# Performance work log

Hardware: AMD Instinct MI355X
Metric: run time of the kernel (lower is better)

## Reference

```python
import jax, jax.numpy as jnp
import numpy as np

WP = 1.0     # warp_penalty
TEMP = 0.01  # soft-min temperature
BIG = 1e7    # finite stand-in for +inf (exp(-BIG/TEMP) == 0 exactly in fp32)


def setup_inputs() -> dict:
    key = jax.random.key(0)
    k1, k2, k3, k4 = jax.random.split(key, 4)
    B, T1, T2, C = 8, 256, 1024, 128
    fea_a = jax.random.normal(k1, (B, T1, C), jnp.float32)
    fea_b = jax.random.normal(k2, (B, T2, C), jnp.float32)
    len_a = jax.random.randint(k3, (B,), T1 // 2, T1 + 1)
    len_b = jax.random.randint(k4, (B,), T2 // 2, T2 + 1)
    return {"fea_a": fea_a, "len_a": len_a, "fea_b": fea_b, "len_b": len_b}


def _softmin(v, temp):
    # v: [3, B, T1]; stable -temp*log(sum(exp(-v/temp)))
    m = jnp.min(v, axis=0)
    return m - temp * jnp.log(jnp.sum(jnp.exp(-(v - m) / temp), axis=0))


def _soft_dtw(fea_a, fea_b, len_a, len_b, wp=WP, temp=TEMP):
    B, T1, C = fea_a.shape
    T2 = fea_b.shape[1]
    # L1 cost: [B, T2, T1]  (rows index fea_b, cols index fea_a, as in torch code)
    cost = jnp.mean(jnp.abs(fea_a[:, None, :, :] - fea_b[:, :, None, :]), axis=-1)
    # skewed cost: skew[b, d, j] = cost[b, clip(d-j, 0, T2-1), j]
    D = T1 + T2 - 1
    d = jnp.arange(D)[:, None]
    j = jnp.arange(T1)[None, :]
    idx = jnp.clip(d - j, 0, T2 - 1)           # [D, T1]
    skew = cost[:, idx, j]                      # [B, D, T1]
    skew = jnp.swapaxes(skew, 0, 1)             # [D, B, T1] for scan

    pc0 = jnp.full((B, T1 + 1), BIG, jnp.float32)       # path_cost (diag d-1)
    pcp0 = pc0.at[:, 0].set(0.0)                         # path_cost_prev (diag d-2)

    def step(carry, crow):
        pc, pcp = carry
        dirs = jnp.stack([pcp[:, :-1], pc[:, 1:] + wp, pc[:, :-1] + wp], axis=0)
        new = crow + _softmin(dirs, temp)                # [B, T1]
        new = jnp.concatenate([jnp.full((B, 1), BIG, new.dtype), new], axis=1)
        return (new, pc), new

    _, ys = jax.lax.scan(step, (pc0, pcp0), skew)        # ys: [D, B, T1+1]
    # per-sample answer: diagonal len_a+len_b-2, entry len_a
    di = len_a + len_b - 2
    loss_i = ys[di, jnp.arange(B), len_a]
    return jnp.sum(loss_i)  # reduction='mean' over a length-1 accumulator == sum


def reference(fea_a, len_a, fea_b, len_b):
    return _soft_dtw(fea_a, fea_b, len_a, len_b)
```

## Files before the change

### kernel.cpp

```cpp
#include <hip/hip_runtime.h>
#include <hip/hip_bf16.h>
#include <hip/hip_fp16.h>
#include <cstddef>
#include <cstdint>

#define BIGV 10000000.0f
#define WPV  1.0f

#define BATCH 8
#define T1N 256
#define T2N 1024
#define CN 128
#define DN 1279

#define RPB 16
#define NSLOT 3
#define SLOT_BYTES (RPB * 1024)
#define FLAG_MAGIC 0x600D0000

typedef __attribute__((ext_vector_type(2))) _Float16 half2v;

__global__ __launch_bounds__(256) void cost_kernel(const float* __restrict__ A,
                                                   const float* __restrict__ Bf,
                                                   const int* __restrict__ lenA,
                                                   const int* __restrict__ lenB,
                                                   float* __restrict__ sk) {
    __shared__ char As[64 * 256];
    __shared__ char Bs[127 * 256];

    const int b  = blockIdx.z;
    const int d0 = blockIdx.y * 64;
    const int j0 = blockIdx.x * 64;
    const int tid = threadIdx.x;

    const int dEnd = lenA[b] + lenB[b] - 2;
    if (d0 > dEnd) return;

    const float* Ab = A  + (size_t)b * T1N * CN;
    const float* Bb = Bf + (size_t)b * T2N * CN;

    const int tj = tid & 15;
    const int td = tid >> 4;
    const int brow0 = td - tj + 63;
    const int rbase = d0 - j0 - 63;

#define SWB(row, g) (((row) << 8) + ((((g) + (row)) & 15) << 4))

    #pragma unroll
    for (int i = 0; i < 8; ++i) {
        int idx = tid + i * 256;
        int row = idx >> 5;
        int q   = idx & 31;
        float4 f = *(const float4*)(Ab + (size_t)(j0 + row) * CN + (q << 2));
        half2v h0 = { (_Float16)f.x, (_Float16)f.y };
        half2v h1 = { (_Float16)f.z, (_Float16)f.w };
        char* dst = As + SWB(row, q >> 1) + ((q & 1) << 3);
        ((uint32_t*)dst)[0] = __builtin_bit_cast(uint32_t, h0);
        ((uint32_t*)dst)[1] = __builtin_bit_cast(uint32_t, h1);
    }
    #pragma unroll
    for (int i = 0; i < 16; ++i) {
        int idx = tid + i * 256;
        if (idx < 4064) {
            int row = idx >> 5;
            int q   = idx & 31;
            int gr = rbase + row;
            gr = gr < 0 ? 0 : (gr > T2N - 1 ? T2N - 1 : gr);
            float4 f = *(const float4*)(Bb + (size_t)gr * CN + (q << 2));
            half2v h0 = { (_Float16)f.x, (_Float16)f.y };
            half2v h1 = { (_Float16)f.z, (_Float16)f.w };
            char* dst = Bs + SWB(row, q >> 1) + ((q & 1) << 3);
            ((uint32_t*)dst)[0] = __builtin_bit_cast(uint32_t, h0);
            ((uint32_t*)dst)[1] = __builtin_bit_cast(uint32_t, h1);
        }
    }
    __syncthreads();

    float acc[4][4];
    #pragma unroll
    for (int i = 0; i < 4; ++i)
        #pragma unroll
        for (int j = 0; j < 4; ++j) acc[i][j] = 0.0f;

    const half2v one2 = { (_Float16)1.0f, (_Float16)1.0f };

    for (int g = 0; g < 16; ++g) {
        uint4 a4[4], bv[7];
        #pragma unroll
        for (int ji = 0; ji < 4; ++ji) {
            int row = tj + 16 * ji;
            a4[ji] = *(const uint4*)(As + SWB(row, g));
        }
        #pragma unroll
        for (int m = 0; m < 7; ++m) {
            int row = brow0 + 16 * (m - 3);
            bv[m] = *(const uint4*)(Bs + SWB(row, g));
        }
        #pragma unroll
        for (int dk = 0; dk < 4; ++dk) {
            #pragma unroll
            for (int ji = 0; ji < 4; ++ji) {
                uint4 au = a4[ji];
                uint4 bu = bv[dk - ji + 3];
                float a = acc[dk][ji];
                #pragma unroll
                for (int w = 0; w < 4; ++w) {
                    uint32_t ua = (&au.x)[w];
                    uint32_t ub = (&bu.x)[w];
                    half2v d2 = __builtin_bit_cast(half2v, ua)
                              - __builtin_bit_cast(half2v, ub);
                    uint32_t du = __builtin_bit_cast(uint32_t, d2) & 0x7FFF7FFFu;
#if __has_builtin(__builtin_amdgcn_fdot2)
                    a = __builtin_amdgcn_fdot2(__builtin_bit_cast(half2v, du),
                                               one2, a, false);
#else
                    half2v ad = __builtin_bit_cast(half2v, du);
                    a += (float)ad.x + (float)ad.y;
#endif
                }
                acc[dk][ji] = a;
            }
        }
    }
#undef SWB

    #pragma unroll
    for (int dk = 0; dk < 4; ++dk) {
        int d = d0 + td + 16 * dk;
        if (d < DN) {
            size_t rowoff = ((size_t)b * DN + d) * T1N;
            #pragma unroll
            for (int ji = 0; ji < 4; ++ji) {
                int j = j0 + tj + 16 * ji;
                sk[rowoff + j] = acc[dk][ji] * (1.0f / 128.0f);
            }
        }
    }
}

__global__ __launch_bounds__(128, 1) void dp_wave_kernel(const float* __restrict__ sk,
                                                         const int* __restrict__ lenA,
                                                         const int* __restrict__ lenB,
                                                         float* __restrict__ partials,
                                                         int* __restrict__ flags,
                                                         float* __restrict__ out) {
    __shared__ char ring[NSLOT * SLOT_BYTES];
    __shared__ int prod_cnt;
    __shared__ int cons_cnt;

    const int b = blockIdx.x;
    if (threadIdx.x == 0) { prod_cnt = 0; cons_cnt = 0; }
    __syncthreads();

    const int wave = threadIdx.x >> 6;
    const int L = threadIdx.x & 63;

    const int la = __builtin_amdgcn_readfirstlane(lenA[b]);
    const int lb = __builtin_amdgcn_readfirstlane(lenB[b]);
    const int dEnd = la + lb - 2;
    const int kLast = dEnd >> 4;
    const int nblk = kLast + 1;

    if (wave == 1) {
        const float* skbp = sk + (size_t)b * DN * T1N + (L << 2);
        for (int k = 0; k < nblk; ++k) {
            if (k >= NSLOT) {
                while (__hip_atomic_load(&cons_cnt, __ATOMIC_ACQUIRE,
                                         __HIP_MEMORY_SCOPE_WORKGROUP) < k - (NSLOT - 1))
                    __builtin_amdgcn_s_sleep(1);
            }
            char* slot = ring + (k % NSLOT) * SLOT_BYTES;
            const int r0 = k * RPB;
            #pragma unroll
            for (int r = 0; r < RPB; ++r) {
                int row = r0 + r; row = row > DN - 1 ? DN - 1 : row;
                __builtin_amdgcn_global_load_lds(
                    (const __attribute__((address_space(1))) void*)(skbp + (size_t)row * T1N),
                    (__attribute__((address_space(3))) void*)(slot + (r << 10)),
                    16, 0, 0);
            }
            asm volatile("s_waitcnt vmcnt(16)" ::: "memory");
            if (L == 0)
                __hip_atomic_store(&prod_cnt, k, __ATOMIC_RELEASE,
                                   __HIP_MEMORY_SCOPE_WORKGROUP);
        }
        asm volatile("s_waitcnt vmcnt(0)" ::: "memory");
        if (L == 0)
            __hip_atomic_store(&prod_cnt, nblk, __ATOMIC_RELEASE,
                               __HIP_MEMORY_SCOPE_WORKGROUP);
        return;
    }

    float v1_0 = BIGV, v1_1 = BIGV, v1_2 = BIGV, v1_3 = BIGV;
    float v2_0 = BIGV, v2_1 = BIGV, v2_2 = BIGV, v2_3 = BIGV;
    float p1_prev = (L == 0) ? 0.0f : BIGV;

#define SHFL_UP1(SRC)                                                       \
    __int_as_float(__builtin_amdgcn_update_dpp(                             \
        __float_as_int(BIGV), __float_as_int(SRC),                          \
        0x138 , 0xF, 0xF, false))

#define DP_STEP(C4) do {                                                    \
        float4 c = (C4);                                                    \
        float p1 = SHFL_UP1(v1_3);                                          \
        float p2 = p1_prev;                                                 \
        float n0 = c.x + fminf(p2,   fminf(v1_0, p1)   + WPV);              \
        float n1 = c.y + fminf(v2_0, fminf(v1_1, v1_0) + WPV);              \
        float n2 = c.z + fminf(v2_1, fminf(v1_2, v1_1) + WPV);              \
        float n3 = c.w + fminf(v2_2, fminf(v1_3, v1_2) + WPV);              \
        p1_prev = p1;                                                       \
        v2_0 = v1_0; v2_1 = v1_1; v2_2 = v1_2; v2_3 = v1_3;                 \
        v1_0 = n0;   v1_1 = n1;   v1_2 = n2;   v1_3 = n3;                   \
    } while (0)

#define DP_STEP_G(C4, R) do {                                               \
        float4 c = (C4);                                                    \
        float p1 = SHFL_UP1(v1_3);                                          \
        float p2 = p1_prev;                                                 \
        float n0 = c.x + fminf(p2,   fminf(v1_0, p1)   + WPV);              \
        float n1 = c.y + fminf(v2_0, fminf(v1_1, v1_0) + WPV);              \
        float n2 = c.z + fminf(v2_1, fminf(v1_2, v1_1) + WPV);              \
        float n3 = c.w + fminf(v2_2, fminf(v1_3, v1_2) + WPV);              \
        if ((R) <= rem) {                                                   \
            p1_prev = p1;                                                   \
            v2_0 = v1_0; v2_1 = v1_1; v2_2 = v1_2; v2_3 = v1_3;             \
            v1_0 = n0;   v1_1 = n1;   v1_2 = n2;   v1_3 = n3;               \
        }                                                                   \
    } while (0)

#define WAIT_BLK(K) do {                                                    \
        while (__hip_atomic_load(&prod_cnt, __ATOMIC_ACQUIRE,               \
                                 __HIP_MEMORY_SCOPE_WORKGROUP) < (K) + 1)   \
            __builtin_amdgcn_s_sleep(1);                                    \
    } while (0)

#define READ_BLK(K)                                                         \
        const char* slot = ring + ((K) % NSLOT) * SLOT_BYTES;               \
        const float4* rp = (const float4*)(slot + (L << 4));                \
        float4 c0  = rp[0 * 64],  c1  = rp[1 * 64],  c2  = rp[2 * 64],  c3  = rp[3 * 64];  \
        float4 c4_ = rp[4 * 64],  c5  = rp[5 * 64],  c6  = rp[6 * 64],  c7  = rp[7 * 64];  \
        float4 c8  = rp[8 * 64],  c9  = rp[9 * 64],  c10 = rp[10 * 64], c11 = rp[11 * 64]; \
        float4 c12 = rp[12 * 64], c13 = rp[13 * 64], c14 = rp[14 * 64], c15 = rp[15 * 64]; \
        __builtin_amdgcn_sched_barrier(0);

    for (int k = 0; k < kLast; ++k) {
        WAIT_BLK(k);
        READ_BLK(k);
        DP_STEP(c0);  DP_STEP(c1);  DP_STEP(c2);  DP_STEP(c3);
        DP_STEP(c4_); DP_STEP(c5);  DP_STEP(c6);  DP_STEP(c7);
        DP_STEP(c8);  DP_STEP(c9);  DP_STEP(c10); DP_STEP(c11);
        DP_STEP(c12); DP_STEP(c13); DP_STEP(c14); DP_STEP(c15);
        if (L == 0)
            __hip_atomic_store(&cons_cnt, k + 1, __ATOMIC_RELEASE,
                               __HIP_MEMORY_SCOPE_WORKGROUP);
    }

    {
        const int rem = dEnd & 15;
        WAIT_BLK(kLast);
        READ_BLK(kLast);
        DP_STEP_G(c0, 0);   DP_STEP_G(c1, 1);   DP_STEP_G(c2, 2);   DP_STEP_G(c3, 3);
        DP_STEP_G(c4_, 4);  DP_STEP_G(c5, 5);   DP_STEP_G(c6, 6);   DP_STEP_G(c7, 7);
        DP_STEP_G(c8, 8);   DP_STEP_G(c9, 9);   DP_STEP_G(c10, 10); DP_STEP_G(c11, 11);
        DP_STEP_G(c12, 12); DP_STEP_G(c13, 13); DP_STEP_G(c14, 14); DP_STEP_G(c15, 15);
    }

    const int tcap = la - 1;
    if (L == (tcap >> 2)) {
        const int k = tcap & 3;
        float r = v1_0;
        if (k == 1) r = v1_1;
        else if (k == 2) r = v1_2;
        else if (k == 3) r = v1_3;
        partials[b] = r;
        __threadfence();
        __hip_atomic_store(&flags[b], FLAG_MAGIC + b,
                           __ATOMIC_RELEASE, __HIP_MEMORY_SCOPE_AGENT);
    }

    if (b == 0 && L == 0) {
        float s = 0.0f;
        for (int i = 0; i < BATCH; ++i) {
            while (__hip_atomic_load(&flags[i], __ATOMIC_ACQUIRE,
                                     __HIP_MEMORY_SCOPE_AGENT) != FLAG_MAGIC + i)
                __builtin_amdgcn_s_sleep(2);
            s += __hip_atomic_load(&partials[i], __ATOMIC_RELAXED,
                                   __HIP_MEMORY_SCOPE_AGENT);
        }
        out[0] = s;
    }
#undef READ_BLK
#undef WAIT_BLK
#undef DP_STEP_G
#undef DP_STEP
#undef SHFL_UP1
}

extern "C" void kernel_launch(void* const* d_in, const int* in_sizes, int n_in,
                              void* d_out, int out_size, void* d_ws, size_t ws_size,
                              hipStream_t stream) {
    const float* feaA = (const float*)d_in[0];
    const int*   lenA = (const int*)d_in[1];
    const float* feaB = (const float*)d_in[2];
    const int*   lenB = (const int*)d_in[3];

    float* sk = (float*)d_ws;
    float* partials = (float*)((char*)d_ws + (size_t)BATCH * DN * T1N * sizeof(float));
    int*   flags    = (int*)(partials + BATCH);

    cost_kernel<<<dim3(T1N / 64, (DN + 63) / 64, BATCH), 256, 0, stream>>>(feaA, feaB, lenA, lenB, sk);
    dp_wave_kernel<<<BATCH, 128, 0, stream>>>(sk, lenA, lenB, partials, flags, (float*)d_out);
}
```

Baseline: 139.8 us.

## Replace LDS producer-consumer ring with register double-buffered prefetch in DP kernel

```diff
diff --git a/kernel.cpp b/kernel.cpp
--- a/kernel.cpp
+++ b/kernel.cpp
@@ -13,9 +13,6 @@
 #define CN 128
 #define DN 1279
 
-#define RPB 16
-#define NSLOT 3
-#define SLOT_BYTES (RPB * 1024)
 #define FLAG_MAGIC 0x600D0000
 
 typedef __attribute__((ext_vector_type(2))) _Float16 half2v;
@@ -138,76 +135,65 @@
     }
 }
 
-__global__ __launch_bounds__(128, 1) void dp_wave_kernel(const float* __restrict__ sk,
-                                                         const int* __restrict__ lenA,
-                                                         const int* __restrict__ lenB,
-                                                         float* __restrict__ partials,
-                                                         int* __restrict__ flags,
-                                                         float* __restrict__ out) {
-    __shared__ char ring[NSLOT * SLOT_BYTES];
-    __shared__ int prod_cnt;
-    __shared__ int cons_cnt;
-
+__device__ __forceinline__ float min3f(float a, float b, float c) {
+    float d;
+    asm("v_min3_f32 %0, %1, %2, %3" : "=v"(d) : "v"(a), "v"(b), "v"(c));
+    return d;
+}
+
+__global__ __launch_bounds__(64, 1) void dp_reg_kernel(const float* __restrict__ sk,
+                                                       const int* __restrict__ lenA,
+                                                       const int* __restrict__ lenB,
+                                                       float* __restrict__ partials,
+                                                       int* __restrict__ flags,
+                                                       float* __restrict__ out) {
     const int b = blockIdx.x;
-    if (threadIdx.x == 0) { prod_cnt = 0; cons_cnt = 0; }
-    __syncthreads();
-
-    const int wave = threadIdx.x >> 6;
-    const int L = threadIdx.x & 63;
+    const int L = threadIdx.x;
 
     const int la = __builtin_amdgcn_readfirstlane(lenA[b]);
     const int lb = __builtin_amdgcn_readfirstlane(lenB[b]);
     const int dEnd = la + lb - 2;
     const int kLast = dEnd >> 4;
-    const int nblk = kLast + 1;
-
-    if (wave == 1) {
-        const float* skbp = sk + (size_t)b * DN * T1N + (L << 2);
-        for (int k = 0; k < nblk; ++k) {
-            if (k >= NSLOT) {
-                while (__hip_atomic_load(&cons_cnt, __ATOMIC_ACQUIRE,
-                                         __HIP_MEMORY_SCOPE_WORKGROUP) < k - (NSLOT - 1))
-                    __builtin_amdgcn_s_sleep(1);
-            }
-            char* slot = ring + (k % NSLOT) * SLOT_BYTES;
-            const int r0 = k * RPB;
-            #pragma unroll
-            for (int r = 0; r < RPB; ++r) {
-                int row = r0 + r; row = row > DN - 1 ? DN - 1 : row;
-                __builtin_amdgcn_global_load_lds(
-                    (const __attribute__((address_space(1))) void*)(skbp + (size_t)row * T1N),
-                    (__attribute__((address_space(3))) void*)(slot + (r << 10)),
-                    16, 0, 0);
-            }
-            asm volatile("s_waitcnt vmcnt(16)" ::: "memory");
-            if (L == 0)
-                __hip_atomic_store(&prod_cnt, k, __ATOMIC_RELEASE,
-                                   __HIP_MEMORY_SCOPE_WORKGROUP);
-        }
-        asm volatile("s_waitcnt vmcnt(0)" ::: "memory");
-        if (L == 0)
-            __hip_atomic_store(&prod_cnt, nblk, __ATOMIC_RELEASE,
-                               __HIP_MEMORY_SCOPE_WORKGROUP);
-        return;
-    }
+
+    const char* lanep = (const char*)(sk + (size_t)b * DN * T1N) + (L << 4);
 
     float v1_0 = BIGV, v1_1 = BIGV, v1_2 = BIGV, v1_3 = BIGV;
     float v2_0 = BIGV, v2_1 = BIGV, v2_2 = BIGV, v2_3 = BIGV;
     float p1_prev = (L == 0) ? 0.0f : BIGV;
+
+    float4 A0, A1, A2, A3, A4, A5, A6, A7, A8, A9, A10, A11, A12, A13, A14, A15;
+    float4 B0, B1, B2, B3, B4, B5, B6, B7, B8, B9, B10, B11, B12, B13, B14, B15;
 
 #define SHFL_UP1(SRC)                                                       \
     __int_as_float(__builtin_amdgcn_update_dpp(                             \
         __float_as_int(BIGV), __float_as_int(SRC),                          \
         0x138 , 0xF, 0xF, false))
 
+#define LOAD1(DST, KB, R) do {                                              \
+        int row_ = ((KB) << 4) + (R);                                       \
+        row_ = row_ > dEnd ? dEnd : row_;                                   \
+        DST = *(const float4*)(lanep + (size_t)row_ * (T1N * 4));           \
+    } while (0)
+
+#define LOADALL(P, KB) do {                                                 \
+        LOAD1(P##0, KB, 0);   LOAD1(P##1, KB, 1);   LOAD1(P##2, KB, 2);     \
+        LOAD1(P##3, KB, 3);   LOAD1(P##4, KB, 4);   LOAD1(P##5, KB, 5);     \
+        LOAD1(P##6, KB, 6);   LOAD1(P##7, KB, 7);   LOAD1(P##8, KB, 8);     \
+        LOAD1(P##9, KB, 9);   LOAD1(P##10, KB, 10); LOAD1(P##11, KB, 11);   \
+        LOAD1(P##12, KB, 12); LOAD1(P##13, KB, 13); LOAD1(P##14, KB, 14);   \
+        LOAD1(P##15, KB, 15);                                               \
+    } while (0)
+
 #define DP_STEP(C4) do {                                                    \
         float4 c = (C4);                                                    \
         float p1 = SHFL_UP1(v1_3);                                          \
-        float p2 = p1_prev;                                                 \
-        float n0 = c.x + fminf(p2,   fminf(v1_0, p1)   + WPV);              \
-        float n1 = c.y + fminf(v2_0, fminf(v1_1, v1_0) + WPV);              \
-        float n2 = c.z + fminf(v2_1, fminf(v1_2, v1_1) + WPV);              \
-        float n3 = c.w + fminf(v2_2, fminf(v1_3, v1_2) + WPV);              \
+        float w0 = v1_0 + WPV, w1 = v1_1 + WPV;                             \
+        float w2 = v1_2 + WPV, w3 = v1_3 + WPV;                             \
+        float wp = p1 + WPV;                                                \
+        float n0 = c.x + min3f(p1_prev, w0, wp);                            \
+        float n1 = c.y + min3f(v2_0, w1, w0);                               \
+        float n2 = c.z + min3f(v2_1, w2, w1);                               \
+        float n3 = c.w + min3f(v2_2, w3, w2);                               \
         p1_prev = p1;                                                       \
         v2_0 = v1_0; v2_1 = v1_1; v2_2 = v1_2; v2_3 = v1_3;                 \
         v1_0 = n0;   v1_1 = n1;   v1_2 = n2;   v1_3 = n3;                   \
@@ -216,11 +202,13 @@
 #define DP_STEP_G(C4, R) do {                                               \
         float4 c = (C4);                                                    \
         float p1 = SHFL_UP1(v1_3);                                          \
-        float p2 = p1_prev;                                                 \
-        float n0 = c.x + fminf(p2,   fminf(v1_0, p1)   + WPV);              \
-        float n1 = c.y + fminf(v2_0, fminf(v1_1, v1_0) + WPV);              \
-        float n2 = c.z + fminf(v2_1, fminf(v1_2, v1_1) + WPV);              \
-        float n3 = c.w + fminf(v2_2, fminf(v1_3, v1_2) + WPV);              \
+        float w0 = v1_0 + WPV, w1 = v1_1 + WPV;                             \
+        float w2 = v1_2 + WPV, w3 = v1_3 + WPV;                             \
+        float wp = p1 + WPV;                                                \
+        float n0 = c.x + min3f(p1_prev, w0, wp);                            \
+        float n1 = c.y + min3f(v2_0, w1, w0);                               \
+        float n2 = c.z + min3f(v2_1, w2, w1);                               \
+        float n3 = c.w + min3f(v2_2, w3, w2);                               \
         if ((R) <= rem) {                                                   \
             p1_prev = p1;                                                   \
             v2_0 = v1_0; v2_1 = v1_1; v2_2 = v1_2; v2_3 = v1_3;             \
@@ -228,50 +216,60 @@
         }                                                                   \
     } while (0)
 
-#define WAIT_BLK(K) do {                                                    \
-        while (__hip_atomic_load(&prod_cnt, __ATOMIC_ACQUIRE,               \
-                                 __HIP_MEMORY_SCOPE_WORKGROUP) < (K) + 1)   \
-            __builtin_amdgcn_s_sleep(1);                                    \
-    } while (0)
-
-#define READ_BLK(K)                                                         \
-        const char* slot = ring + ((K) % NSLOT) * SLOT_BYTES;               \
-        const float4* rp = (const float4*)(slot + (L << 4));                \
-        float4 c0  = rp[0 * 64],  c1  = rp[1 * 64],  c2  = rp[2 * 64],  c3  = rp[3 * 64];  \
-        float4 c4_ = rp[4 * 64],  c5  = rp[5 * 64],  c6  = rp[6 * 64],  c7  = rp[7 * 64];  \
-        float4 c8  = rp[8 * 64],  c9  = rp[9 * 64],  c10 = rp[10 * 64], c11 = rp[11 * 64]; \
-        float4 c12 = rp[12 * 64], c13 = rp[13 * 64], c14 = rp[14 * 64], c15 = rp[15 * 64]; \
-        __builtin_amdgcn_sched_barrier(0);
-
-    for (int k = 0; k < kLast; ++k) {
-        WAIT_BLK(k);
-        READ_BLK(k);
-        DP_STEP(c0);  DP_STEP(c1);  DP_STEP(c2);  DP_STEP(c3);
-        DP_STEP(c4_); DP_STEP(c5);  DP_STEP(c6);  DP_STEP(c7);
-        DP_STEP(c8);  DP_STEP(c9);  DP_STEP(c10); DP_STEP(c11);
-        DP_STEP(c12); DP_STEP(c13); DP_STEP(c14); DP_STEP(c15);
-        if (L == 0)
-            __hip_atomic_store(&cons_cnt, k + 1, __ATOMIC_RELEASE,
-                               __HIP_MEMORY_SCOPE_WORKGROUP);
-    }
-
-    {
+#define STEP_RL(C4, KB, R) do { DP_STEP(C4); LOAD1(C4, KB, R); } while (0)
+
+#define PROC_RELOAD(P, KB) do {                                             \
+        STEP_RL(P##0, KB, 0);   STEP_RL(P##1, KB, 1);                       \
+        STEP_RL(P##2, KB, 2);   STEP_RL(P##3, KB, 3);                       \
+        STEP_RL(P##4, KB, 4);   STEP_RL(P##5, KB, 5);                       \
+        STEP_RL(P##6, KB, 6);   STEP_RL(P##7, KB, 7);                       \
+        STEP_RL(P##8, KB, 8);   STEP_RL(P##9, KB, 9);                       \
+        STEP_RL(P##10, KB, 10); STEP_RL(P##11, KB, 11);                     \
+        STEP_RL(P##12, KB, 12); STEP_RL(P##13, KB, 13);                     \
+        STEP_RL(P##14, KB, 14); STEP_RL(P##15, KB, 15);                     \
+    } while (0)
+
+#define PROC_FULL(P) do {                                                   \
+        DP_STEP(P##0);  DP_STEP(P##1);  DP_STEP(P##2);  DP_STEP(P##3);      \
+        DP_STEP(P##4);  DP_STEP(P##5);  DP_STEP(P##6);  DP_STEP(P##7);      \
+        DP_STEP(P##8);  DP_STEP(P##9);  DP_STEP(P##10); DP_STEP(P##11);     \
+        DP_STEP(P##12); DP_STEP(P##13); DP_STEP(P##14); DP_STEP(P##15);     \
+    } while (0)
+
+#define PROC_GUARD(P) do {                                                  \
+        DP_STEP_G(P##0, 0);   DP_STEP_G(P##1, 1);   DP_STEP_G(P##2, 2);     \
+        DP_STEP_G(P##3, 3);   DP_STEP_G(P##4, 4);   DP_STEP_G(P##5, 5);     \
+        DP_STEP_G(P##6, 6);   DP_STEP_G(P##7, 7);   DP_STEP_G(P##8, 8);     \
+        DP_STEP_G(P##9, 9);   DP_STEP_G(P##10, 10); DP_STEP_G(P##11, 11);   \
+        DP_STEP_G(P##12, 12); DP_STEP_G(P##13, 13); DP_STEP_G(P##14, 14);   \
+        DP_STEP_G(P##15, 15);                                               \
+    } while (0)
+
+    LOADALL(A, 0);
+    LOADALL(B, 1);
+
+    int k = 0;
+    while (k + 1 < kLast) {
+        PROC_RELOAD(A, k + 2);
+        PROC_RELOAD(B, k + 3);
+        k += 2;
+    }
+    if (k < kLast) {
+        PROC_FULL(A);
         const int rem = dEnd & 15;
-        WAIT_BLK(kLast);
-        READ_BLK(kLast);
-        DP_STEP_G(c0, 0);   DP_STEP_G(c1, 1);   DP_STEP_G(c2, 2);   DP_STEP_G(c3, 3);
-        DP_STEP_G(c4_, 4);  DP_STEP_G(c5, 5);   DP_STEP_G(c6, 6);   DP_STEP_G(c7, 7);
-        DP_STEP_G(c8, 8);   DP_STEP_G(c9, 9);   DP_STEP_G(c10, 10); DP_STEP_G(c11, 11);
-        DP_STEP_G(c12, 12); DP_STEP_G(c13, 13); DP_STEP_G(c14, 14); DP_STEP_G(c15, 15);
+        PROC_GUARD(B);
+    } else {
+        const int rem = dEnd & 15;
+        PROC_GUARD(A);
     }
 
     const int tcap = la - 1;
     if (L == (tcap >> 2)) {
-        const int k = tcap & 3;
+        const int kk = tcap & 3;
         float r = v1_0;
-        if (k == 1) r = v1_1;
-        else if (k == 2) r = v1_2;
-        else if (k == 3) r = v1_3;
+        if (kk == 1) r = v1_1;
+        else if (kk == 2) r = v1_2;
+        else if (kk == 3) r = v1_3;
         partials[b] = r;
         __threadfence();
         __hip_atomic_store(&flags[b], FLAG_MAGIC + b,
@@ -289,10 +287,14 @@
         }
         out[0] = s;
     }
-#undef READ_BLK
-#undef WAIT_BLK
+#undef PROC_GUARD
+#undef PROC_FULL
+#undef PROC_RELOAD
+#undef STEP_RL
 #undef DP_STEP_G
 #undef DP_STEP
+#undef LOADALL
+#undef LOAD1
 #undef SHFL_UP1
 }
 
@@ -309,5 +311,5 @@
     int*   flags    = (int*)(partials + BATCH);
 
     cost_kernel<<<dim3(T1N / 64, (DN + 63) / 64, BATCH), 256, 0, stream>>>(feaA, feaB, lenA, lenB, sk);
-    dp_wave_kernel<<<BATCH, 128, 0, stream>>>(sk, lenA, lenB, partials, flags, (float*)d_out);
+    dp_reg_kernel<<<BATCH, 64, 0, stream>>>(sk, lenA, lenB, partials, flags, (float*)d_out);
 }
```

New measurement: 137.0 us, median of 2. 1.02x faster.
